# Optimization experiments

Hardware: AMD Instinct MI355X
Metric: run time of the kernel (lower is better)

The kernel has to match this reference:

```python
import jax, jax.numpy as jnp
import numpy as np
import math


def _packet_loss_to_partial_patch(x, loss_rate):
    # Zero out randomly-chosen 1472-byte chunks of the NHWC-flattened tensor,
    # exactly mirroring the torch loop but as one vectorized masked multiply.
    B, C, H, W = x.shape
    xp = jnp.transpose(x, (0, 2, 3, 1)).reshape(-1)  # NHWC flatten
    n = xp.shape[0]
    elem_size = 4  # float32 bytes
    elems_per_chunk = 1472 // elem_size  # 368
    num_chunks = math.ceil(n * elem_size / 1472)
    num_lossy = int(math.ceil(num_chunks * (loss_rate / 100)))
    perm = jax.random.permutation(jax.random.key(1234), num_chunks)
    keep = jnp.ones((num_chunks,), xp.dtype).at[perm[:num_lossy]].set(0.0)
    elem_keep = jnp.repeat(keep, elems_per_chunk)[:n]
    xp = xp * elem_keep
    return jnp.transpose(xp.reshape(B, H, W, C), (0, 3, 1, 2))


def setup_inputs() -> dict:
    key = jax.random.key(0)
    ks = jax.random.split(key, 7)
    B, C, H, W = 32, 256, 56, 56
    r = 16
    s = 0.05
    return {
        "x": jax.random.normal(ks[0], (B, C, H, W), jnp.float32),
        "fc1_w": jax.random.normal(ks[1], (C // r, C), jnp.float32) * s,
        "fc2_w": jax.random.normal(ks[2], (C, C // r), jnp.float32) * s,
        "threshold": jnp.array([0.5], jnp.float32),
        "detect_w": jax.random.normal(ks[3], (C, C), jnp.float32) * s,
        "rec1_w": jax.random.normal(ks[4], (C, 2 * C), jnp.float32) * s,
        "rec2_w": jax.random.normal(ks[5], (C, C), jnp.float32) * s,
        "adapt_w": jax.random.normal(ks[6], (C, 1), jnp.float32) * s,
        "Packet_Loss_Rate": 50,
    }


def reference(x, fc1_w, fc2_w, threshold, detect_w, rec1_w, rec2_w, adapt_w, Packet_Loss_Rate):
    x = _packet_loss_to_partial_patch(x, Packet_Loss_Rate)
    B, C, H, W = x.shape
    # SE channel attention
    y = jnp.mean(x, axis=(2, 3))                              # [B, C]
    scores = jax.nn.sigmoid(jax.nn.relu(y @ fc1_w.T) @ fc2_w.T)  # [B, C]
    # packet-loss adaptation: Linear(1 -> C) applied to rate*ones([B,1])
    adapt = jnp.asarray(Packet_Loss_Rate, x.dtype) * adapt_w[:, 0]  # [C]
    mask = jax.nn.relu(scores + adapt[None, :] - threshold)   # [B, C]
    mask = mask[:, :, None, None]
    # 1x1 convs as channel GEMMs
    det = jnp.einsum('oc,bchw->bohw', detect_w, x)
    z = jnp.concatenate([x, jax.nn.sigmoid(det) * x], axis=1)  # [B, 2C, H, W]
    r = jax.nn.relu(jnp.einsum('oc,bchw->bohw', rec1_w, z))
    r = jnp.einsum('oc,bchw->bohw', rec2_w, r)
    return r * mask
```

## Files before the change

kernel.cpp:

```cpp
#include <hip/hip_runtime.h>
#include <stdint.h>

#define PARTITIONABLE 1

typedef float f32x4 __attribute__((ext_vector_type(4)));
typedef short bf16x8 __attribute__((ext_vector_type(8)));

namespace {
constexpr int Hh = 56, Ww = 56;
constexpr int HW = Hh * Ww;
constexpr int Bsz = 32, Cch = 256;
constexpr int NCH = 69811;
constexpr int HALF = 34906;
constexpr int NB2 = 4096;

constexpr int SC1_W   = 0;
constexpr int SC2_W   = 139648;
constexpr int BITS1_W = 279296;
constexpr int BITS2_W = 349120;
constexpr int R1_W    = 418944;
constexpr int R2_W    = 488768;
constexpr int HIST1_W = 558592;
constexpr int PRE1_W  = 562688;
constexpr int CNT1_W  = 566784;
constexpr int HIST2_W = 570880;
constexpr int PRE2_W  = 574976;
constexpr int CNT2_W  = 579072;
constexpr int Y_W     = 583168;

constexpr int KEEP_W  = 0;
constexpr int MASKV_W = 69824;
constexpr int WPACK_W = 78016;
}

__host__ __device__ constexpr uint32_t rotl32(uint32_t v, int r) {
  return (v << r) | (v >> (32 - r));
}
__host__ __device__ constexpr uint64_t tf2x32(uint32_t k0, uint32_t k1,
                                              uint32_t x0, uint32_t x1) {
  uint32_t ks2 = k0 ^ k1 ^ 0x1BD11BDAu;
  x0 += k0; x1 += k1;
  {const int R[4]={13,15,26,6};  for(int i=0;i<4;i++){x0+=x1;x1=rotl32(x1,R[i]);x1^=x0;}}
  x0 += k1;  x1 += ks2 + 1u;
  {const int R[4]={17,29,16,24}; for(int i=0;i<4;i++){x0+=x1;x1=rotl32(x1,R[i]);x1^=x0;}}
  x0 += ks2; x1 += k0 + 2u;
  {const int R[4]={13,15,26,6};  for(int i=0;i<4;i++){x0+=x1;x1=rotl32(x1,R[i]);x1^=x0;}}
  x0 += k0;  x1 += k1 + 3u;
  {const int R[4]={17,29,16,24}; for(int i=0;i<4;i++){x0+=x1;x1=rotl32(x1,R[i]);x1^=x0;}}
  x0 += k1;  x1 += ks2 + 4u;
  {const int R[4]={13,15,26,6};  for(int i=0;i<4;i++){x0+=x1;x1=rotl32(x1,R[i]);x1^=x0;}}
  x0 += ks2; x1 += k0 + 5u;
  return ((uint64_t)x0 << 32) | x1;
}

#if PARTITIONABLE
constexpr uint64_t KEY1 = tf2x32(0u, 1234u, 0u, 0u);
constexpr uint64_t SUB1 = tf2x32(0u, 1234u, 0u, 1u);
constexpr uint64_t SUB2 = tf2x32((uint32_t)(KEY1 >> 32), (uint32_t)KEY1, 0u, 1u);
constexpr uint32_t S1H = (uint32_t)(SUB1 >> 32), S1L = (uint32_t)SUB1;
constexpr uint32_t S2H = (uint32_t)(SUB2 >> 32), S2L = (uint32_t)SUB2;
#else
constexpr uint64_t E0 = tf2x32(0u, 1234u, 0u, 2u);
constexpr uint64_t E1 = tf2x32(0u, 1234u, 1u, 3u);
constexpr uint32_t K1H = (uint32_t)(E0 >> 32), K1L = (uint32_t)(E1 >> 32);
constexpr uint64_t F0 = tf2x32(K1H, K1L, 0u, 2u);
constexpr uint64_t F1 = tf2x32(K1H, K1L, 1u, 3u);
constexpr uint32_t S1H = (uint32_t)E0, S1L = (uint32_t)E1;
constexpr uint32_t S2H = (uint32_t)F0, S2L = (uint32_t)F1;
#endif

__device__ __forceinline__ uint32_t rnd_bits(uint32_t kh, uint32_t kl, uint32_t i) {
#if PARTITIONABLE
  uint64_t r = tf2x32(kh, kl, 0u, i);
  return (uint32_t)(r >> 32) ^ (uint32_t)r;
#else
  if (i < (uint32_t)HALF) {
    uint32_t x1 = (i + HALF < (uint32_t)NCH) ? i + HALF : 0u;
    return (uint32_t)(tf2x32(kh, kl, i, x1) >> 32);
  } else {
    return (uint32_t)tf2x32(kh, kl, i - HALF, i);
  }
#endif
}

__device__ __forceinline__ uint32_t f2bf(float f) {
  uint32_t u = __float_as_uint(f);
  return (u + 0x7FFFu + ((u >> 16) & 1u)) >> 16;
}
__device__ __forceinline__ float bf2f(uint32_t h) {
  return __uint_as_float(h << 16);
}
__device__ __forceinline__ uint32_t cvtpk(float lo, float hi) {
  uint32_t r;
  asm("v_cvt_pk_bf16_f32 %0, %1, %2" : "=v"(r) : "v"(lo), "v"(hi));
  return r;
}

__global__ void k_bits(uint32_t* bits1, uint32_t* bits2,
                       uint32_t* hist1, uint32_t* hist2) {
  int i = blockIdx.x * 256 + threadIdx.x;
  if (i >= NCH) return;
  uint32_t b1 = rnd_bits(S1H, S1L, (uint32_t)i);
  uint32_t b2 = rnd_bits(S2H, S2L, (uint32_t)i);
  bits1[i] = b1; bits2[i] = b2;
  atomicAdd(&hist1[b1 >> 20], 1u);
  atomicAdd(&hist2[b2 >> 20], 1u);
}

__global__ __launch_bounds__(1024) void k_scan2(const uint32_t* h1, uint32_t* p1o,
                                                const uint32_t* h2, uint32_t* p2o) {
  const uint32_t* h = blockIdx.x ? h2 : h1;
  uint32_t* pre = blockIdx.x ? p2o : p1o;
  __shared__ uint32_t part[1024];
  int t = threadIdx.x;
  uint4 v = *(const uint4*)&h[t * 4];
  uint32_t s = v.x + v.y + v.z + v.w;
  part[t] = s;
  __syncthreads();
  for (int off = 1; off < 1024; off <<= 1) {
    uint32_t u = (t >= off) ? part[t - off] : 0u;
    __syncthreads();
    part[t] += u;
    __syncthreads();
  }
  uint32_t run = part[t] - s;
  uint4 o;
  o.x = run; o.y = run + v.x; o.z = o.y + v.y; o.w = o.z + v.z;
  *(uint4*)&pre[t * 4] = o;
}

__global__ void k_scatter2(const uint32_t* bits1, const uint32_t* pre1,
                           uint32_t* cnt1, uint64_t* sc1,
                           const uint32_t* bits2, const uint32_t* pre2,
                           uint32_t* cnt2, uint64_t* sc2) {
  int blk = blockIdx.x;
  bool second = blk >= 273;
  const uint32_t* bits = second ? bits2 : bits1;
  const uint32_t* pre  = second ? pre2  : pre1;
  uint32_t* cnt = second ? cnt2 : cnt1;
  uint64_t* sc  = second ? sc2  : sc1;
  int i = (second ? blk - 273 : blk) * 256 + threadIdx.x;
  if (i >= NCH) return;
  uint32_t b = bits[i], bk = b >> 20;
  uint32_t pos = pre[bk] + atomicAdd(&cnt[bk], 1u);
  sc[pos] = ((uint64_t)b << 32) | (uint32_t)i;
}

__global__ void k_rank2(const uint32_t* bits1, const uint32_t* pre1,
                        const uint32_t* hist1, const uint64_t* sc1, uint32_t* rk1,
                        const uint32_t* bits2, const uint32_t* pre2,
                        const uint32_t* hist2, const uint64_t* sc2, uint32_t* rk2) {
  int blk = blockIdx.x;
  bool second = blk >= 273;
  const uint32_t* bits = second ? bits2 : bits1;
  const uint32_t* pre  = second ? pre2  : pre1;
  const uint32_t* hist = second ? hist2 : hist1;
  const uint64_t* sc   = second ? sc2   : sc1;
  uint32_t* rnk = second ? rk2 : rk1;
  int i = (second ? blk - 273 : blk) * 256 + threadIdx.x;
  if (i >= NCH) return;
  uint32_t b = bits[i], bk = b >> 20;
  uint32_t s = pre[bk], n = hist[bk];
  uint64_t my = ((uint64_t)b << 32) | (uint32_t)i;
  uint32_t c = 0;
  for (uint32_t k = 0; k < n; ++k) c += (sc[s + k] < my) ? 1u : 0u;
  rnk[i] = s + c;
}

__global__ void k_keepwpack(const uint32_t* r1, const uint32_t* r2,
                            const int* plr, float* keep,
                            const float* __restrict__ dw,
                            const float* __restrict__ r1w,
                            const float* __restrict__ r2w,
                            ushort* __restrict__ wdp, ushort* __restrict__ w1p,
                            ushort* __restrict__ w2p) {
  int blk = blockIdx.x;
  if (blk < 273) {
    int j = blk * 256 + threadIdx.x;
    if (j >= NCH) return;
    int L = (NCH * plr[0] + 99) / 100;
    keep[j] = (r2[r1[j]] < (uint32_t)L) ? 0.f : 1.f;
    return;
  }
  int tid = (blk - 273) * 256 + threadIdx.x;
  const float* src;
  ushort* dst;
  if (tid < 8192) {
    int s = tid, ot = s >> 9, ks = (s >> 6) & 7, l = s & 63;
    src = dw + (ot * 16 + (l & 15)) * 256 + ks * 32 + (l >> 4) * 8;
    dst = wdp + s * 8;
  } else if (tid < 24576) {
    int s = tid - 8192, ot = s >> 10, ks = (s >> 6) & 15, l = s & 63;
    src = r1w + (ot * 16 + (l & 15)) * 512 + ks * 32 + (l >> 4) * 8;
    dst = w1p + s * 8;
  } else {
    int s = tid - 24576, ot = s >> 9, ks = (s >> 6) & 7, l = s & 63;
    src = r2w + (ot * 16 + (l & 15)) * 256 + ks * 32 + (l >> 4) * 8;
    dst = w2p + s * 8;
  }
  float4 v0 = *(const float4*)src;
  float4 v1 = *(const float4*)(src + 4);
  uint4 pk;
  pk.x = f2bf(v0.x) | (f2bf(v0.y) << 16);
  pk.y = f2bf(v0.z) | (f2bf(v0.w) << 16);
  pk.z = f2bf(v1.x) | (f2bf(v1.y) << 16);
  pk.w = f2bf(v1.z) | (f2bf(v1.w) << 16);
  *(uint4*)dst = pk;
}

__global__ void k_ymean(const float* __restrict__ x, const float* __restrict__ keep,
                        float* __restrict__ y) {
  int bc = blockIdx.x;
  int b = bc >> 8, c = bc & 255;
  const float4* row = (const float4*)(x + (size_t)bc * HW);
  int t = threadIdx.x;
  float s = 0.f;
  for (int q = t; q < HW / 4; q += 256) {
    float4 v = row[q];
    uint32_t base = (uint32_t)((b * HW + q * 4) * 256 + c);
    s += v.x * keep[base / 368u];
    s += v.y * keep[(base + 256u) / 368u];
    s += v.z * keep[(base + 512u) / 368u];
    s += v.w * keep[(base + 768u) / 368u];
  }
  for (int off = 32; off > 0; off >>= 1) s += __shfl_down(s, off);
  __shared__ float w4[4];
  if ((t & 63) == 0) w4[t >> 6] = s;
  __syncthreads();
  if (t == 0) y[bc] = (w4[0] + w4[1] + w4[2] + w4[3]) * (1.0f / HW);
}

__global__ void k_scores(const float* __restrict__ y, const float* __restrict__ fc1,
                         const float* __restrict__ fc2, const float* __restrict__ thr,
                         const float* __restrict__ aw, const int* __restrict__ plr,
                         float* __restrict__ maskv) {
  int b = blockIdx.x, t = threadIdx.x;
  __shared__ float ysh[256];
  __shared__ float hsh[16];
  ysh[t] = y[b * 256 + t];
  __syncthreads();
  if (t < 16) {
    float a = 0.f;
    for (int c = 0; c < 256; ++c) a += ysh[c] * fc1[t * 256 + c];
    hsh[t] = fmaxf(a, 0.f);
  }
  __syncthreads();
  float s = 0.f;
  #pragma unroll
  for (int j = 0; j < 16; ++j) s += hsh[j] * fc2[t * 16 + j];
  float sc = 1.f / (1.f + expf(-s));
  float m = sc + (float)plr[0] * aw[t] - thr[0];
  maskv[b * 256 + t] = fmaxf(m, 0.f);
}

__global__ __launch_bounds__(512, 4) void k_main(
    const float* __restrict__ x, const float* __restrict__ keep,
    const ushort* __restrict__ wdp, const ushort* __restrict__ w1p,
    const ushort* __restrict__ w2p, const float* __restrict__ maskv,
    float* __restrict__ out) {
  __shared__ __align__(16) short XT[16384];
  __shared__ __align__(16) short ST[16384];
  int tile = blockIdx.x;
  int bb = tile / 49, hw0 = (tile % 49) * 64;
  int t = threadIdx.x;
  int lane = t & 63, w = t >> 6;
  int l15 = lane & 15, lhi = lane >> 4;

  {
    const float* xb = x + (size_t)bb * (Cch * HW);
    uint32_t pixb = (uint32_t)(bb * HW + hw0);
    int p = lane;
    uint32_t ia0 = (pixb + (uint32_t)p) * 256u;
    uint32_t k0 = ia0 / 368u;
    uint32_t cstar = 368u * (k0 + 1u) - ia0;
    float kp0 = keep[k0];
    float kp1 = keep[k0 + 1];
    const float* xcol = xb + hw0 + p;
    int c0 = w * 32;
    #pragma unroll
    for (int k = 0; k < 4; ++k) {
      uint32_t pw0, pw1, pw2, pw3;
      #pragma unroll
      for (int h = 0; h < 4; ++h) {
        uint32_t ca = (uint32_t)(c0 + k * 8 + h * 2);
        float va = xcol[(size_t)ca * HW] * (ca < cstar ? kp0 : kp1);
        float vb = xcol[(size_t)(ca + 1u) * HW] * ((ca + 1u) < cstar ? kp0 : kp1);
        uint32_t pkv = cvtpk(va, vb);
        if (h == 0) pw0 = pkv; else if (h == 1) pw1 = pkv;
        else if (h == 2) pw2 = pkv; else pw3 = pkv;
      }
      uint4 pk; pk.x = pw0; pk.y = pw1; pk.z = pw2; pk.w = pw3;
      *(uint4*)&XT[(w * 4 + (p >> 4)) * 512 + ((p & 15) + 16 * k) * 8] = pk;
    }
  }
  __syncthreads();

  f32x4 zero4 = {0.f, 0.f, 0.f, 0.f};
  f32x4 acc[2][4];
  int row16a = (lhi >> 1);
  int sub4 = (lhi & 1) * 4;

  #pragma unroll
  for (int mt = 0; mt < 2; ++mt)
    #pragma unroll
    for (int nt = 0; nt < 4; ++nt) acc[mt][nt] = zero4;
  {
    const ushort* a0p = wdp + ((w * 2 + 0) * 8) * 512 + lane * 8;
    const ushort* a1p = wdp + ((w * 2 + 1) * 8) * 512 + lane * 8;
    bf16x8 A0[8], A1[8];
    #pragma unroll
    for (int k = 0; k < 8; ++k) {
      A0[k] = *(const bf16x8*)(a0p + k * 512);
      A1[k] = *(const bf16x8*)(a1p + k * 512);
    }
    #pragma unroll
    for (int ks = 0; ks < 8; ++ks) {
      #pragma unroll
      for (int nt = 0; nt < 4; ++nt) {
        bf16x8 b = *(const bf16x8*)&XT[(ks * 4 + nt) * 512 + lane * 8];
        acc[0][nt] = __builtin_amdgcn_mfma_f32_16x16x32_bf16(A0[ks], b, acc[0][nt], 0, 0, 0);
        acc[1][nt] = __builtin_amdgcn_mfma_f32_16x16x32_bf16(A1[ks], b, acc[1][nt], 0, 0, 0);
      }
    }
  }

  #pragma unroll
  for (int mt = 0; mt < 2; ++mt) {
    int row16 = mt * 2 + row16a;
    #pragma unroll
    for (int nt = 0; nt < 4; ++nt) {
      int off = (w * 4 + nt) * 512 + (l15 + 16 * row16) * 8 + sub4;
      ushort4 xv = *(const ushort4*)&XT[off];
      float s0 = bf2f(xv.x) / (1.f + __expf(-acc[mt][nt][0]));
      float s1 = bf2f(xv.y) / (1.f + __expf(-acc[mt][nt][1]));
      float s2 = bf2f(xv.z) / (1.f + __expf(-acc[mt][nt][2]));
      float s3 = bf2f(xv.w) / (1.f + __expf(-acc[mt][nt][3]));
      uint2 sv;
      sv.x = cvtpk(s0, s1);
      sv.y = cvtpk(s2, s3);
      *(uint2*)&ST[off] = sv;
    }
  }
  __syncthreads();

  f32x4 acc2[2][4];
  #pragma unroll
  for (int mt = 0; mt < 2; ++mt)
    #pragma unroll
    for (int nt = 0; nt < 4; ++nt) acc2[mt][nt] = zero4;
  {
    const ushort* a0p = w1p + ((w * 2 + 0) * 16) * 512 + lane * 8;
    const ushort* a1p = w1p + ((w * 2 + 1) * 16) * 512 + lane * 8;
    bf16x8 A0[8], A1[8];
    #pragma unroll
    for (int k = 0; k < 8; ++k) {
      A0[k] = *(const bf16x8*)(a0p + k * 512);
      A1[k] = *(const bf16x8*)(a1p + k * 512);
    }
    #pragma unroll
    for (int ks = 0; ks < 8; ++ks) {
      #pragma unroll
      for (int nt = 0; nt < 4; ++nt) {
        bf16x8 b = *(const bf16x8*)&XT[(ks * 4 + nt) * 512 + lane * 8];
        acc2[0][nt] = __builtin_amdgcn_mfma_f32_16x16x32_bf16(A0[ks], b, acc2[0][nt], 0, 0, 0);
        acc2[1][nt] = __builtin_amdgcn_mfma_f32_16x16x32_bf16(A1[ks], b, acc2[1][nt], 0, 0, 0);
      }
    }
    #pragma unroll
    for (int k = 0; k < 8; ++k) {
      A0[k] = *(const bf16x8*)(a0p + (k + 8) * 512);
      A1[k] = *(const bf16x8*)(a1p + (k + 8) * 512);
    }
    #pragma unroll
    for (int ks = 0; ks < 8; ++ks) {
      #pragma unroll
      for (int nt = 0; nt < 4; ++nt) {
        bf16x8 b = *(const bf16x8*)&ST[(ks * 4 + nt) * 512 + lane * 8];
        acc2[0][nt] = __builtin_amdgcn_mfma_f32_16x16x32_bf16(A0[ks], b, acc2[0][nt], 0, 0, 0);
        acc2[1][nt] = __builtin_amdgcn_mfma_f32_16x16x32_bf16(A1[ks], b, acc2[1][nt], 0, 0, 0);
      }
    }
  }
  __syncthreads();

  #pragma unroll
  for (int mt = 0; mt < 2; ++mt) {
    int row16 = mt * 2 + row16a;
    #pragma unroll
    for (int nt = 0; nt < 4; ++nt) {
      int off = (w * 4 + nt) * 512 + (l15 + 16 * row16) * 8 + sub4;
      uint2 rv;
      rv.x = cvtpk(fmaxf(acc2[mt][nt][0], 0.f), fmaxf(acc2[mt][nt][1], 0.f));
      rv.y = cvtpk(fmaxf(acc2[mt][nt][2], 0.f), fmaxf(acc2[mt][nt][3], 0.f));
      *(uint2*)&XT[off] = rv;
    }
  }
  __syncthreads();

  #pragma unroll
  for (int mt = 0; mt < 2; ++mt)
    #pragma unroll
    for (int nt = 0; nt < 4; ++nt) acc[mt][nt] = zero4;
  {
    const ushort* a0p = w2p + ((w * 2 + 0) * 8) * 512 + lane * 8;
    const ushort* a1p = w2p + ((w * 2 + 1) * 8) * 512 + lane * 8;
    bf16x8 A0[8], A1[8];
    #pragma unroll
    for (int k = 0; k < 8; ++k) {
      A0[k] = *(const bf16x8*)(a0p + k * 512);
      A1[k] = *(const bf16x8*)(a1p + k * 512);
    }
    #pragma unroll
    for (int ks = 0; ks < 8; ++ks) {
      #pragma unroll
      for (int nt = 0; nt < 4; ++nt) {
        bf16x8 b = *(const bf16x8*)&XT[(ks * 4 + nt) * 512 + lane * 8];
        acc[0][nt] = __builtin_amdgcn_mfma_f32_16x16x32_bf16(A0[ks], b, acc[0][nt], 0, 0, 0);
        acc[1][nt] = __builtin_amdgcn_mfma_f32_16x16x32_bf16(A1[ks], b, acc[1][nt], 0, 0, 0);
      }
    }
  }

  #pragma unroll
  for (int mt = 0; mt < 2; ++mt)
    #pragma unroll
    for (int r = 0; r < 4; ++r) {
      int o = w * 32 + mt * 16 + 4 * lhi + r;
      float m = maskv[bb * 256 + o];
      float* orow = out + (size_t)(bb * 256 + o) * HW + hw0;
      #pragma unroll
      for (int nt = 0; nt < 4; ++nt)
        orow[nt * 16 + l15] = acc[mt][nt][r] * m;
    }
}

extern "C" void kernel_launch(void* const* d_in, const int* in_sizes, int n_in,
                              void* d_out, int out_size, void* d_ws, size_t ws_size,
                              hipStream_t stream) {
  const float* x   = (const float*)d_in[0];
  const float* fc1 = (const float*)d_in[1];
  const float* fc2 = (const float*)d_in[2];
  const float* thr = (const float*)d_in[3];
  const float* dw  = (const float*)d_in[4];
  const float* r1w = (const float*)d_in[5];
  const float* r2w = (const float*)d_in[6];
  const float* aw  = (const float*)d_in[7];
  const int*   plr = (const int*)d_in[8];

  float*    out = (float*)d_out;
  uint32_t* ob  = (uint32_t*)d_out;
  float*    ws  = (float*)d_ws;

  uint64_t* sc1   = (uint64_t*)(ob + SC1_W);
  uint64_t* sc2   = (uint64_t*)(ob + SC2_W);
  uint32_t* bits1 = ob + BITS1_W;
  uint32_t* bits2 = ob + BITS2_W;
  uint32_t* rk1   = ob + R1_W;
  uint32_t* rk2   = ob + R2_W;
  uint32_t* hist1 = ob + HIST1_W;
  uint32_t* pre1  = ob + PRE1_W;
  uint32_t* cnt1  = ob + CNT1_W;
  uint32_t* hist2 = ob + HIST2_W;
  uint32_t* pre2  = ob + PRE2_W;
  uint32_t* cnt2  = ob + CNT2_W;
  float*    yv    = (float*)(ob + Y_W);

  float*  keep  = ws + KEEP_W;
  float*  maskv = ws + MASKV_W;
  ushort* wdp   = (ushort*)(ws + WPACK_W);
  ushort* w1p   = wdp + 65536;
  ushort* w2p   = w1p + 131072;

  hipMemsetAsync((void*)(ob + HIST1_W), 0, (size_t)6 * NB2 * 4, stream);

  dim3 blk(256);
  k_bits<<<273, blk, 0, stream>>>(bits1, bits2, hist1, hist2);
  k_scan2<<<2, 1024, 0, stream>>>(hist1, pre1, hist2, pre2);
  k_scatter2<<<546, blk, 0, stream>>>(bits1, pre1, cnt1, sc1,
                                      bits2, pre2, cnt2, sc2);
  k_rank2<<<546, blk, 0, stream>>>(bits1, pre1, hist1, sc1, rk1,
                                   bits2, pre2, hist2, sc2, rk2);
  k_keepwpack<<<401, blk, 0, stream>>>(rk1, rk2, plr, keep, dw, r1w, r2w,
                                       wdp, w1p, w2p);
  k_ymean<<<8192, blk, 0, stream>>>(x, keep, yv);
  k_scores<<<32, blk, 0, stream>>>(yv, fc1, fc2, thr, aw, plr, maskv);
  k_main<<<1568, 512, 0, stream>>>(x, keep, wdp, w1p, w2p, maskv, out);
}
```

Before: 149.2 us.

## Drop second LDS buffer and stream weight fragments to raise occupancy

Removes the separate ST shared buffer by keeping the sigmoid-gated tile in registers. The gated tile is written back into XT only after the first half of the rec1 GEMM has finished reading x. Weight fragments are now loaded per k-step instead of prefetched as eight-deep arrays. Launch bounds go from 4 to 6 blocks per CU. The aim is to halve LDS use and cut register pressure so more waves are resident, at the cost of an extra barrier and less load latency hiding for the weight reads.

```diff
diff --git a/kernel.cpp b/kernel.cpp
--- a/kernel.cpp
+++ b/kernel.cpp
@@ -253,13 +253,12 @@
   maskv[b * 256 + t] = fmaxf(m, 0.f);
 }
 
-__global__ __launch_bounds__(512, 4) void k_main(
+__global__ __launch_bounds__(512, 6) void k_main(
     const float* __restrict__ x, const float* __restrict__ keep,
     const ushort* __restrict__ wdp, const ushort* __restrict__ w1p,
     const ushort* __restrict__ w2p, const float* __restrict__ maskv,
     float* __restrict__ out) {
   __shared__ __align__(16) short XT[16384];
-  __shared__ __align__(16) short ST[16384];
   int tile = blockIdx.x;
   int bb = tile / 49, hw0 = (tile % 49) * 64;
   int t = threadIdx.x;
@@ -307,23 +306,20 @@
   {
     const ushort* a0p = wdp + ((w * 2 + 0) * 8) * 512 + lane * 8;
     const ushort* a1p = wdp + ((w * 2 + 1) * 8) * 512 + lane * 8;
-    bf16x8 A0[8], A1[8];
-    #pragma unroll
-    for (int k = 0; k < 8; ++k) {
-      A0[k] = *(const bf16x8*)(a0p + k * 512);
-      A1[k] = *(const bf16x8*)(a1p + k * 512);
-    }
     #pragma unroll
     for (int ks = 0; ks < 8; ++ks) {
+      bf16x8 a0 = *(const bf16x8*)(a0p + ks * 512);
+      bf16x8 a1 = *(const bf16x8*)(a1p + ks * 512);
       #pragma unroll
       for (int nt = 0; nt < 4; ++nt) {
         bf16x8 b = *(const bf16x8*)&XT[(ks * 4 + nt) * 512 + lane * 8];
-        acc[0][nt] = __builtin_amdgcn_mfma_f32_16x16x32_bf16(A0[ks], b, acc[0][nt], 0, 0, 0);
-        acc[1][nt] = __builtin_amdgcn_mfma_f32_16x16x32_bf16(A1[ks], b, acc[1][nt], 0, 0, 0);
+        acc[0][nt] = __builtin_amdgcn_mfma_f32_16x16x32_bf16(a0, b, acc[0][nt], 0, 0, 0);
+        acc[1][nt] = __builtin_amdgcn_mfma_f32_16x16x32_bf16(a1, b, acc[1][nt], 0, 0, 0);
       }
     }
   }
 
+  uint2 strg[2][4];
   #pragma unroll
   for (int mt = 0; mt < 2; ++mt) {
     int row16 = mt * 2 + row16a;
@@ -335,13 +331,10 @@
       float s1 = bf2f(xv.y) / (1.f + __expf(-acc[mt][nt][1]));
       float s2 = bf2f(xv.z) / (1.f + __expf(-acc[mt][nt][2]));
       float s3 = bf2f(xv.w) / (1.f + __expf(-acc[mt][nt][3]));
-      uint2 sv;
-      sv.x = cvtpk(s0, s1);
-      sv.y = cvtpk(s2, s3);
-      *(uint2*)&ST[off] = sv;
-    }
-  }
-  __syncthreads();
+      strg[mt][nt].x = cvtpk(s0, s1);
+      strg[mt][nt].y = cvtpk(s2, s3);
+    }
+  }
 
   f32x4 acc2[2][4];
   #pragma unroll
@@ -351,33 +344,43 @@
   {
     const ushort* a0p = w1p + ((w * 2 + 0) * 16) * 512 + lane * 8;
     const ushort* a1p = w1p + ((w * 2 + 1) * 16) * 512 + lane * 8;
-    bf16x8 A0[8], A1[8];
-    #pragma unroll
-    for (int k = 0; k < 8; ++k) {
-      A0[k] = *(const bf16x8*)(a0p + k * 512);
-      A1[k] = *(const bf16x8*)(a1p + k * 512);
-    }
     #pragma unroll
     for (int ks = 0; ks < 8; ++ks) {
+      bf16x8 a0 = *(const bf16x8*)(a0p + ks * 512);
+      bf16x8 a1 = *(const bf16x8*)(a1p + ks * 512);
       #pragma unroll
       for (int nt = 0; nt < 4; ++nt) {
         bf16x8 b = *(const bf16x8*)&XT[(ks * 4 + nt) * 512 + lane * 8];
-        acc2[0][nt] = __builtin_amdgcn_mfma_f32_16x16x32_bf16(A0[ks], b, acc2[0][nt], 0, 0, 0);
-        acc2[1][nt] = __builtin_amdgcn_mfma_f32_16x16x32_bf16(A1[ks], b, acc2[1][nt], 0, 0, 0);
+        acc2[0][nt] = __builtin_amdgcn_mfma_f32_16x16x32_bf16(a0, b, acc2[0][nt], 0, 0, 0);
+        acc2[1][nt] = __builtin_amdgcn_mfma_f32_16x16x32_bf16(a1, b, acc2[1][nt], 0, 0, 0);
       }
     }
-    #pragma unroll
-    for (int k = 0; k < 8; ++k) {
-      A0[k] = *(const bf16x8*)(a0p + (k + 8) * 512);
-      A1[k] = *(const bf16x8*)(a1p + (k + 8) * 512);
-    }
+  }
+  __syncthreads();
+
+  #pragma unroll
+  for (int mt = 0; mt < 2; ++mt) {
+    int row16 = mt * 2 + row16a;
+    #pragma unroll
+    for (int nt = 0; nt < 4; ++nt) {
+      int off = (w * 4 + nt) * 512 + (l15 + 16 * row16) * 8 + sub4;
+      *(uint2*)&XT[off] = strg[mt][nt];
+    }
+  }
+  __syncthreads();
+
+  {
+    const ushort* a0p = w1p + ((w * 2 + 0) * 16 + 8) * 512 + lane * 8;
+    const ushort* a1p = w1p + ((w * 2 + 1) * 16 + 8) * 512 + lane * 8;
     #pragma unroll
     for (int ks = 0; ks < 8; ++ks) {
+      bf16x8 a0 = *(const bf16x8*)(a0p + ks * 512);
+      bf16x8 a1 = *(const bf16x8*)(a1p + ks * 512);
       #pragma unroll
       for (int nt = 0; nt < 4; ++nt) {
-        bf16x8 b = *(const bf16x8*)&ST[(ks * 4 + nt) * 512 + lane * 8];
-        acc2[0][nt] = __builtin_amdgcn_mfma_f32_16x16x32_bf16(A0[ks], b, acc2[0][nt], 0, 0, 0);
-        acc2[1][nt] = __builtin_amdgcn_mfma_f32_16x16x32_bf16(A1[ks], b, acc2[1][nt], 0, 0, 0);
+        bf16x8 b = *(const bf16x8*)&XT[(ks * 4 + nt) * 512 + lane * 8];
+        acc2[0][nt] = __builtin_amdgcn_mfma_f32_16x16x32_bf16(a0, b, acc2[0][nt], 0, 0, 0);
+        acc2[1][nt] = __builtin_amdgcn_mfma_f32_16x16x32_bf16(a1, b, acc2[1][nt], 0, 0, 0);
       }
     }
   }
@@ -404,19 +407,15 @@
   {
     const ushort* a0p = w2p + ((w * 2 + 0) * 8) * 512 + lane * 8;
     const ushort* a1p = w2p + ((w * 2 + 1) * 8) * 512 + lane * 8;
-    bf16x8 A0[8], A1[8];
-    #pragma unroll
-    for (int k = 0; k < 8; ++k) {
-      A0[k] = *(const bf16x8*)(a0p + k * 512);
-      A1[k] = *(const bf16x8*)(a1p + k * 512);
-    }
     #pragma unroll
     for (int ks = 0; ks < 8; ++ks) {
+      bf16x8 a0 = *(const bf16x8*)(a0p + ks * 512);
+      bf16x8 a1 = *(const bf16x8*)(a1p + ks * 512);
       #pragma unroll
       for (int nt = 0; nt < 4; ++nt) {
         bf16x8 b = *(const bf16x8*)&XT[(ks * 4 + nt) * 512 + lane * 8];
-        acc[0][nt] = __builtin_amdgcn_mfma_f32_16x16x32_bf16(A0[ks], b, acc[0][nt], 0, 0, 0);
-        acc[1][nt] = __builtin_amdgcn_mfma_f32_16x16x32_bf16(A1[ks], b, acc[1][nt], 0, 0, 0);
+        acc[0][nt] = __builtin_amdgcn_mfma_f32_16x16x32_bf16(a0, b, acc[0][nt], 0, 0, 0);
+        acc[1][nt] = __builtin_amdgcn_mfma_f32_16x16x32_bf16(a1, b, acc[1][nt], 0, 0, 0);
       }
     }
   }
```

New measurement: 362.7 us. 143% more time.

## Fuse detect GEMM with first half of rec1 GEMM sharing XT B-fragments

Applied to the files above, without the earlier changes.

The detect-weight GEMM and the x-half of the rec1 GEMM now run in one loop, so each XT B-fragment is read from LDS once and fed to four MFMAs instead of being loaded twice. The syncthreads before the rec1 ReLU writeback is dropped, and A-fragment loads move inside the ks loop instead of being preloaded into 8-element register arrays. Launch bounds drop from 4 to 2 blocks per CU to make room for the extra live accumulators. The cost is lower occupancy, and the removed barrier may let some waves overwrite XT while others are still reading it.

```diff
diff --git a/kernel.cpp b/kernel.cpp
--- a/kernel.cpp
+++ b/kernel.cpp
@@ -253,7 +253,7 @@
   maskv[b * 256 + t] = fmaxf(m, 0.f);
 }
 
-__global__ __launch_bounds__(512, 4) void k_main(
+__global__ __launch_bounds__(512, 2) void k_main(
     const float* __restrict__ x, const float* __restrict__ keep,
     const ushort* __restrict__ wdp, const ushort* __restrict__ w1p,
     const ushort* __restrict__ w2p, const float* __restrict__ maskv,
@@ -297,29 +297,32 @@
 
   f32x4 zero4 = {0.f, 0.f, 0.f, 0.f};
   f32x4 acc[2][4];
+  f32x4 acc2[2][4];
   int row16a = (lhi >> 1);
   int sub4 = (lhi & 1) * 4;
 
   #pragma unroll
   for (int mt = 0; mt < 2; ++mt)
     #pragma unroll
-    for (int nt = 0; nt < 4; ++nt) acc[mt][nt] = zero4;
+    for (int nt = 0; nt < 4; ++nt) { acc[mt][nt] = zero4; acc2[mt][nt] = zero4; }
   {
-    const ushort* a0p = wdp + ((w * 2 + 0) * 8) * 512 + lane * 8;
-    const ushort* a1p = wdp + ((w * 2 + 1) * 8) * 512 + lane * 8;
-    bf16x8 A0[8], A1[8];
-    #pragma unroll
-    for (int k = 0; k < 8; ++k) {
-      A0[k] = *(const bf16x8*)(a0p + k * 512);
-      A1[k] = *(const bf16x8*)(a1p + k * 512);
-    }
+    const ushort* d0p = wdp + ((w * 2 + 0) * 8) * 512 + lane * 8;
+    const ushort* d1p = wdp + ((w * 2 + 1) * 8) * 512 + lane * 8;
+    const ushort* e0p = w1p + ((w * 2 + 0) * 16) * 512 + lane * 8;
+    const ushort* e1p = w1p + ((w * 2 + 1) * 16) * 512 + lane * 8;
     #pragma unroll
     for (int ks = 0; ks < 8; ++ks) {
+      bf16x8 ad0 = *(const bf16x8*)(d0p + ks * 512);
+      bf16x8 ad1 = *(const bf16x8*)(d1p + ks * 512);
+      bf16x8 ae0 = *(const bf16x8*)(e0p + ks * 512);
+      bf16x8 ae1 = *(const bf16x8*)(e1p + ks * 512);
       #pragma unroll
       for (int nt = 0; nt < 4; ++nt) {
         bf16x8 b = *(const bf16x8*)&XT[(ks * 4 + nt) * 512 + lane * 8];
-        acc[0][nt] = __builtin_amdgcn_mfma_f32_16x16x32_bf16(A0[ks], b, acc[0][nt], 0, 0, 0);
-        acc[1][nt] = __builtin_amdgcn_mfma_f32_16x16x32_bf16(A1[ks], b, acc[1][nt], 0, 0, 0);
+        acc[0][nt]  = __builtin_amdgcn_mfma_f32_16x16x32_bf16(ad0, b, acc[0][nt], 0, 0, 0);
+        acc[1][nt]  = __builtin_amdgcn_mfma_f32_16x16x32_bf16(ad1, b, acc[1][nt], 0, 0, 0);
+        acc2[0][nt] = __builtin_amdgcn_mfma_f32_16x16x32_bf16(ae0, b, acc2[0][nt], 0, 0, 0);
+        acc2[1][nt] = __builtin_amdgcn_mfma_f32_16x16x32_bf16(ae1, b, acc2[1][nt], 0, 0, 0);
       }
     }
   }
@@ -343,45 +346,21 @@
   }
   __syncthreads();
 
-  f32x4 acc2[2][4];
-  #pragma unroll
-  for (int mt = 0; mt < 2; ++mt)
-    #pragma unroll
-    for (int nt = 0; nt < 4; ++nt) acc2[mt][nt] = zero4;
   {
-    const ushort* a0p = w1p + ((w * 2 + 0) * 16) * 512 + lane * 8;
-    const ushort* a1p = w1p + ((w * 2 + 1) * 16) * 512 + lane * 8;
-    bf16x8 A0[8], A1[8];
-    #pragma unroll
-    for (int k = 0; k < 8; ++k) {
-      A0[k] = *(const bf16x8*)(a0p + k * 512);
-      A1[k] = *(const bf16x8*)(a1p + k * 512);
-    }
+    const ushort* e0p = w1p + ((w * 2 + 0) * 16 + 8) * 512 + lane * 8;
+    const ushort* e1p = w1p + ((w * 2 + 1) * 16 + 8) * 512 + lane * 8;
     #pragma unroll
     for (int ks = 0; ks < 8; ++ks) {
-      #pragma unroll
-      for (int nt = 0; nt < 4; ++nt) {
-        bf16x8 b = *(const bf16x8*)&XT[(ks * 4 + nt) * 512 + lane * 8];
-        acc2[0][nt] = __builtin_amdgcn_mfma_f32_16x16x32_bf16(A0[ks], b, acc2[0][nt], 0, 0, 0);
-        acc2[1][nt] = __builtin_amdgcn_mfma_f32_16x16x32_bf16(A1[ks], b, acc2[1][nt], 0, 0, 0);
-      }
-    }
-    #pragma unroll
-    for (int k = 0; k < 8; ++k) {
-      A0[k] = *(const bf16x8*)(a0p + (k + 8) * 512);
-      A1[k] = *(const bf16x8*)(a1p + (k + 8) * 512);
-    }
-    #pragma unroll
-    for (int ks = 0; ks < 8; ++ks) {
+      bf16x8 ae0 = *(const bf16x8*)(e0p + ks * 512);
+      bf16x8 ae1 = *(const bf16x8*)(e1p + ks * 512);
       #pragma unroll
       for (int nt = 0; nt < 4; ++nt) {
         bf16x8 b = *(const bf16x8*)&ST[(ks * 4 + nt) * 512 + lane * 8];
-        acc2[0][nt] = __builtin_amdgcn_mfma_f32_16x16x32_bf16(A0[ks], b, acc2[0][nt], 0, 0, 0);
-        acc2[1][nt] = __builtin_amdgcn_mfma_f32_16x16x32_bf16(A1[ks], b, acc2[1][nt], 0, 0, 0);
+        acc2[0][nt] = __builtin_amdgcn_mfma_f32_16x16x32_bf16(ae0, b, acc2[0][nt], 0, 0, 0);
+        acc2[1][nt] = __builtin_amdgcn_mfma_f32_16x16x32_bf16(ae1, b, acc2[1][nt], 0, 0, 0);
       }
     }
   }
-  __syncthreads();
 
   #pragma unroll
   for (int mt = 0; mt < 2; ++mt) {
@@ -404,19 +383,15 @@
   {
     const ushort* a0p = w2p + ((w * 2 + 0) * 8) * 512 + lane * 8;
     const ushort* a1p = w2p + ((w * 2 + 1) * 8) * 512 + lane * 8;
-    bf16x8 A0[8], A1[8];
-    #pragma unroll
-    for (int k = 0; k < 8; ++k) {
-      A0[k] = *(const bf16x8*)(a0p + k * 512);
-      A1[k] = *(const bf16x8*)(a1p + k * 512);
-    }
     #pragma unroll
     for (int ks = 0; ks < 8; ++ks) {
+      bf16x8 a0 = *(const bf16x8*)(a0p + ks * 512);
+      bf16x8 a1 = *(const bf16x8*)(a1p + ks * 512);
       #pragma unroll
       for (int nt = 0; nt < 4; ++nt) {
         bf16x8 b = *(const bf16x8*)&XT[(ks * 4 + nt) * 512 + lane * 8];
-        acc[0][nt] = __builtin_amdgcn_mfma_f32_16x16x32_bf16(A0[ks], b, acc[0][nt], 0, 0, 0);
-        acc[1][nt] = __builtin_amdgcn_mfma_f32_16x16x32_bf16(A1[ks], b, acc[1][nt], 0, 0, 0);
+        acc[0][nt] = __builtin_amdgcn_mfma_f32_16x16x32_bf16(a0, b, acc[0][nt], 0, 0, 0);
+        acc[1][nt] = __builtin_amdgcn_mfma_f32_16x16x32_bf16(a1, b, acc[1][nt], 0, 0, 0);
       }
     }
   }
```

Result: slower. 172.9 us (+15.9%).
